# Optimization experiments

Measured on AMD Instinct MI355X. Metric: run time of the kernel, lower is better.

The kernel has to match this reference:

```python
import jax, jax.numpy as jnp
import numpy as np

B, C, H, W = 4, 256, 64, 64

def setup_inputs() -> dict:
    key = jax.random.key(0)
    k1, k2, k3, k4, k5, k6 = jax.random.split(key, 6)
    input_1 = jax.random.normal(k1, (B, C, H, W), dtype=jnp.float32)
    input_2 = jax.random.normal(k2, (B, C, H, W), dtype=jnp.float32)
    W_e = jax.random.normal(k3, (C, C), dtype=jnp.float32) * 0.02   # linear_e weight [out,in]
    gate_w = jax.random.normal(k4, (C,), dtype=jnp.float32) * 0.01  # Conv2d(c,1,1) weight squeezed
    W1 = jax.random.normal(k5, (C, 2 * C), dtype=jnp.float32) * 0.01  # final_conv_1 1x1 weight [out,in]
    W2 = jax.random.normal(k6, (C, 2 * C), dtype=jnp.float32) * 0.01  # final_conv_2
    return {"input_1": input_1, "input_2": input_2, "W_e": W_e,
            "gate_w": gate_w, "W1": W1, "W2": W2}

def reference(input_1, input_2, W_e, gate_w, W1, W2):
    b, c, h, w = input_1.shape
    hw = h * w
    ex = input_1.reshape(b, c, hw)   # exemplar_flat (b,c,n)
    q = input_2.reshape(b, c, hw)    # query_flat    (b,c,m)
    # linear_e on exemplar^T: (b,n,c) @ W_e^T -> (b,n,c)
    ec = jnp.einsum('bcn,dc->bnd', ex, W_e)
    # correlation A: (b,n,m)
    A = jnp.einsum('bnd,bdm->bnm', ec, q)
    A1 = jax.nn.softmax(A, axis=1)                       # softmax over exemplar pixels n
    Bmat = jax.nn.softmax(jnp.swapaxes(A, 1, 2), axis=1)  # (b,m,n), softmax over query pixels m
    query_att = jnp.einsum('bcn,bnm->bcm', ex, A1).reshape(b, c, h, w)
    exemplar_att = jnp.einsum('bcm,bmn->bcn', q, Bmat).reshape(b, c, h, w)
    # gate: 1x1 conv to 1 channel + sigmoid + elementwise mul
    m1 = jax.nn.sigmoid(jnp.einsum('bchw,c->bhw', exemplar_att, gate_w))[:, None]
    m2 = jax.nn.sigmoid(jnp.einsum('bchw,c->bhw', query_att, gate_w))[:, None]
    att1 = jnp.concatenate([exemplar_att * m1, input_1], axis=1)  # (b,2c,h,w)
    att2 = jnp.concatenate([query_att * m2, input_2], axis=1)
    out1 = jnp.einsum('bkhw,ok->bohw', att1, W1)
    out2 = jnp.einsum('bkhw,ok->bohw', att2, W2)
    return out1, out2
```

## Files before the change

kernel.cpp:

```cpp
#include <hip/hip_runtime.h>
#include <cstdint>
#include <cstddef>

#define BATCH 4
#define CCH   256
#define HW    4096
#define NM    4096

typedef __attribute__((ext_vector_type(8))) short s16x8;
typedef __attribute__((ext_vector_type(4))) float f32x4;

__device__ __forceinline__ short f2bf(float f) {
    unsigned u = __float_as_uint(f);
    u += 0x7FFFu + ((u >> 16) & 1u);
    return (short)(u >> 16);
}
__device__ __forceinline__ float bf2f(short s) {
    return __uint_as_float(((unsigned)(unsigned short)s) << 16);
}

__global__ __launch_bounds__(256) void k_cast(const float* __restrict__ s,
                                              short* __restrict__ d, int n) {
    int i = (blockIdx.x * 256 + threadIdx.x) * 4;
    if (i + 3 < n) {
        float4 v = *(const float4*)&s[i];
        *(short4*)&d[i] = make_short4(f2bf(v.x), f2bf(v.y), f2bf(v.z), f2bf(v.w));
    }
}

__global__ __launch_bounds__(256) void k_prep(const float* __restrict__ in1,
                                              const float* __restrict__ in2,
                                              short* __restrict__ X16,
                                              short* __restrict__ Q16,
                                              short* __restrict__ Xt16,
                                              short* __restrict__ Qt16) {
    __shared__ short S[64][72];
    int t = threadIdx.x;
    int p0 = blockIdx.x * 64, c0 = blockIdx.y * 64;
    int z = blockIdx.z;
    int b = z >> 1, which = z & 1;
    const float* src = (which ? in2 : in1) + (size_t)b * CCH * HW;
    short* direct = (which ? Q16 : X16) + (size_t)b * CCH * HW;
    short* trans  = (which ? Qt16 : Xt16) + (size_t)b * HW * CCH;
    int tx = t & 15, ty = t >> 4;
#pragma unroll
    for (int i = 0; i < 4; ++i) {
        int c = ty + i * 16;
        float4 v = *(const float4*)&src[(size_t)(c0 + c) * HW + p0 + tx * 4];
        short4 h = make_short4(f2bf(v.x), f2bf(v.y), f2bf(v.z), f2bf(v.w));
        *(short4*)&direct[(size_t)(c0 + c) * HW + p0 + tx * 4] = h;
        S[tx * 4 + 0][c] = h.x;
        S[tx * 4 + 1][c] = h.y;
        S[tx * 4 + 2][c] = h.z;
        S[tx * 4 + 3][c] = h.w;
    }
    __syncthreads();
#pragma unroll
    for (int i = 0; i < 4; ++i) {
        int p = ty + i * 16;
        short4 v = *(const short4*)&S[p][tx * 4];
        *(short4*)&trans[(size_t)(p0 + p) * CCH + c0 + tx * 4] = v;
    }
}

__global__ __launch_bounds__(256) void k_E_mfma(const short* __restrict__ Xt16,
                                                const short* __restrict__ We16,
                                                short* __restrict__ E16n) {
    __shared__ short As[128 * 72];
    __shared__ short Bs[128 * 72];
    int t = threadIdx.x;
    int d0 = blockIdx.x * 128, n0 = blockIdx.y * 128, b = blockIdx.z;
    const short* Xb = Xt16 + (size_t)b * HW * CCH;
    short* Eb = E16n + (size_t)b * HW * CCH;
    int lm = t & 15, q = (t >> 4) & 3, w = t >> 6;
    int wr = (w >> 1) * 64, wc = (w & 1) * 64;
    f32x4 acc[4][4];
#pragma unroll
    for (int i = 0; i < 4; ++i)
#pragma unroll
        for (int j = 0; j < 4; ++j) acc[i][j] = (f32x4){0.f, 0.f, 0.f, 0.f};

    for (int k0 = 0; k0 < CCH; k0 += 64) {
#pragma unroll
        for (int u = 0; u < 4; ++u) {
            int chunk = t + u * 256;
            int row = chunk >> 3, off = (chunk & 7) * 8;
            *(float4*)&As[row * 72 + off] =
                *(const float4*)&Xb[(size_t)(n0 + row) * CCH + k0 + off];
            *(float4*)&Bs[row * 72 + off] =
                *(const float4*)&We16[(size_t)(d0 + row) * CCH + k0 + off];
        }
        __syncthreads();
#pragma unroll
        for (int kk = 0; kk < 2; ++kk) {
            s16x8 af[4], bfr[4];
#pragma unroll
            for (int i = 0; i < 4; ++i)
                af[i] = *(const s16x8*)&As[(wr + i * 16 + lm) * 72 + kk * 32 + q * 8];
#pragma unroll
            for (int j = 0; j < 4; ++j)
                bfr[j] = *(const s16x8*)&Bs[(wc + j * 16 + lm) * 72 + kk * 32 + q * 8];
#pragma unroll
            for (int i = 0; i < 4; ++i)
#pragma unroll
                for (int j = 0; j < 4; ++j)
                    acc[i][j] = __builtin_amdgcn_mfma_f32_16x16x32_bf16(
                        af[i], bfr[j], acc[i][j], 0, 0, 0);
        }
        __syncthreads();
    }
#pragma unroll
    for (int i = 0; i < 4; ++i)
#pragma unroll
        for (int r = 0; r < 4; ++r) {
            size_t base = (size_t)(n0 + wr + i * 16 + q * 4 + r) * CCH;
#pragma unroll
            for (int j = 0; j < 4; ++j)
                Eb[base + d0 + wc + j * 16 + lm] = f2bf(acc[i][j][r]);
        }
}

__global__ __launch_bounds__(512, 2) void k_fused(const short* __restrict__ E16n,
                                                  const short* __restrict__ Qt16,
                                                  const short* __restrict__ Q16,
                                                  const short* __restrict__ X16,
                                                  const float* __restrict__ gw,
                                                  short* __restrict__ eattT,
                                                  short* __restrict__ qattT,
                                                  float* __restrict__ m1v,
                                                  float* __restrict__ m2v) {
    __shared__ short ArS[128 * 264];
    __shared__ short Ps[2][128 * 136];
    __shared__ float rs[8 * 128];
    __shared__ float grs[8 * 128];

    int t = threadIdx.x;
    int gid = blockIdx.x;
    int unit = gid & 7;
    int b = unit >> 1, which = unit & 1;
    int r0 = (gid >> 3) * 128;

    const short* Ar = (which ? Qt16 : E16n) + (size_t)b * HW * CCH;
    const short* Ac = (which ? E16n : Qt16) + (size_t)b * HW * CCH;
    const short* V  = (which ? X16  : Q16 ) + (size_t)b * CCH * HW;
    short* Out = (which ? qattT : eattT) + (size_t)b * HW * CCH;
    float* mdst = (which ? m2v : m1v) + (size_t)b * HW;

    int lm = t & 15, q = (t >> 4) & 3, w = t >> 6;
    int wqs = w * 16;
    int cq  = w * 32;

    float gwv[2];
#pragma unroll
    for (int j = 0; j < 2; ++j) gwv[j] = gw[cq + j * 16 + lm];

#pragma unroll
    for (int u = 0; u < 8; ++u) {
        int chunk = t + u * 512;
        int row = chunk >> 5, off = (chunk & 31) * 8;
        *(float4*)&ArS[row * 264 + off] =
            *(const float4*)&Ar[(size_t)(r0 + row) * CCH + off];
    }
    __syncthreads();

    f32x4 oacc[8][2];
    float rsum[8][4];
#pragma unroll
    for (int i = 0; i < 8; ++i) {
#pragma unroll
        for (int j = 0; j < 2; ++j) oacc[i][j] = (f32x4){0.f, 0.f, 0.f, 0.f};
#pragma unroll
        for (int r = 0; r < 4; ++r) rsum[i][r] = 0.f;
    }

    int buf = 0;
    for (int col0 = 0; col0 < NM; col0 += 128, buf ^= 1) {
        f32x4 sacc[8];
#pragma unroll
        for (int i = 0; i < 8; ++i) sacc[i] = (f32x4){0.f, 0.f, 0.f, 0.f};
#pragma unroll
        for (int kk = 0; kk < 8; ++kk) {
            s16x8 af[8], bf;
#pragma unroll
            for (int i = 0; i < 8; ++i)
                af[i] = *(const s16x8*)&ArS[(i * 16 + lm) * 264 + kk * 32 + q * 8];
            bf = *(const s16x8*)&Ac[(size_t)(col0 + wqs + lm) * CCH + kk * 32 + q * 8];
#pragma unroll
            for (int i = 0; i < 8; ++i)
                sacc[i] = __builtin_amdgcn_mfma_f32_16x16x32_bf16(
                    af[i], bf, sacc[i], 0, 0, 0);
        }
#pragma unroll
        for (int i = 0; i < 8; ++i)
#pragma unroll
            for (int r = 0; r < 4; ++r) {
                float v = bf2f(f2bf(__expf(sacc[i][r])));
                rsum[i][r] += v;
                sacc[i][r] = v;
            }
#pragma unroll
        for (int i = 0; i < 8; ++i)
#pragma unroll
            for (int r = 0; r < 4; ++r)
                Ps[buf][(i * 16 + q * 4 + r) * 136 + wqs + lm] =
                    (short)(__float_as_uint(sacc[i][r]) >> 16);
        __syncthreads();
#pragma unroll
        for (int km = 0; km < 4; ++km) {
            s16x8 pf[8], vf[2];
#pragma unroll
            for (int j = 0; j < 2; ++j)
                vf[j] = *(const s16x8*)&V[(size_t)(cq + j * 16 + lm) * HW +
                                          col0 + km * 32 + q * 8];
#pragma unroll
            for (int i = 0; i < 8; ++i)
                pf[i] = *(const s16x8*)&Ps[buf][(i * 16 + lm) * 136 + km * 32 + q * 8];
#pragma unroll
            for (int i = 0; i < 8; ++i)
#pragma unroll
                for (int j = 0; j < 2; ++j)
                    oacc[i][j] = __builtin_amdgcn_mfma_f32_16x16x32_bf16(
                        pf[i], vf[j], oacc[i][j], 0, 0, 0);
        }
    }

#pragma unroll
    for (int i = 0; i < 8; ++i)
#pragma unroll
        for (int r = 0; r < 4; ++r) {
            float s = rsum[i][r];
            s += __shfl_xor(s, 1, 64);
            s += __shfl_xor(s, 2, 64);
            s += __shfl_xor(s, 4, 64);
            s += __shfl_xor(s, 8, 64);
            if (lm == 0) rs[w * 128 + i * 16 + q * 4 + r] = s;
        }
    __syncthreads();

    float gacc[8][4];
#pragma unroll
    for (int i = 0; i < 8; ++i)
#pragma unroll
        for (int r = 0; r < 4; ++r) {
            int row = i * 16 + q * 4 + r;
            float tot = 0.f;
#pragma unroll
            for (int ww = 0; ww < 8; ++ww) tot += rs[ww * 128 + row];
            float inv = 1.f / tot;
            size_t base = (size_t)(r0 + row) * CCH;
            float ga = 0.f;
#pragma unroll
            for (int j = 0; j < 2; ++j) {
                short h = f2bf(oacc[i][j][r] * inv);
                Out[base + cq + j * 16 + lm] = h;
                ga = fmaf(bf2f(h), gwv[j], ga);
            }
            gacc[i][r] = ga;
        }
#pragma unroll
    for (int i = 0; i < 8; ++i)
#pragma unroll
        for (int r = 0; r < 4; ++r) {
            float s = gacc[i][r];
            s += __shfl_xor(s, 1, 64);
            s += __shfl_xor(s, 2, 64);
            s += __shfl_xor(s, 4, 64);
            s += __shfl_xor(s, 8, 64);
            if (lm == 0) grs[w * 128 + i * 16 + q * 4 + r] = s;
        }
    __syncthreads();
    if (t < 128) {
        float g = 0.f;
#pragma unroll
        for (int ww = 0; ww < 8; ++ww) g += grs[ww * 128 + t];
        mdst[r0 + t] = 1.f / (1.f + __expf(-g));
    }
}

__global__ __launch_bounds__(256) void k_final(const short* __restrict__ W16_1,
                                               const short* __restrict__ W16_2,
                                               const short* __restrict__ eattT,
                                               const short* __restrict__ qattT,
                                               const short* __restrict__ Xt16,
                                               const short* __restrict__ Qt16,
                                               const float* __restrict__ m1v,
                                               const float* __restrict__ m2v,
                                               float* __restrict__ outbase) {
    __shared__ short As[128 * 40];
    __shared__ short Bs[64 * 40];
    int t = threadIdx.x;
    int zz = blockIdx.z;
    int half = zz >> 2, b = zz & 3;
    const short* W16 = half ? W16_2 : W16_1;
    const short* attT = (half ? qattT : eattT);
    const short* inT  = (half ? Qt16 : Xt16);
    const float* gate = half ? m2v : m1v;
    float* outp = outbase + (size_t)half * BATCH * CCH * HW;
    int p0 = blockIdx.x * 64, o0 = blockIdx.y * 128;
    const short* Tb0 = attT + (size_t)b * HW * CCH;
    const short* Tb1 = inT + (size_t)b * HW * CCH;
    int lm = t & 15, q = (t >> 4) & 3, w = t >> 6;
    int wr = (w >> 1) * 64, wc = (w & 1) * 32;
    f32x4 acc[2][4][2];
#pragma unroll
    for (int ph = 0; ph < 2; ++ph)
#pragma unroll
        for (int i = 0; i < 4; ++i)
#pragma unroll
            for (int j = 0; j < 2; ++j) acc[ph][i][j] = (f32x4){0.f, 0.f, 0.f, 0.f};

    int brow = t >> 2, boff = (t & 3) * 8;
    for (int ph = 0; ph < 2; ++ph) {
        const short* Tb = ph ? Tb1 : Tb0;
        for (int k0 = 0; k0 < CCH; k0 += 32) {
#pragma unroll
            for (int u = 0; u < 2; ++u) {
                int chunk = t + u * 256;
                int row = chunk >> 2, off = (chunk & 3) * 8;
                *(float4*)&As[row * 40 + off] =
                    *(const float4*)&W16[(size_t)(o0 + row) * 512 + ph * 256 + k0 + off];
            }
            *(float4*)&Bs[brow * 40 + boff] =
                *(const float4*)&Tb[(size_t)(p0 + brow) * CCH + k0 + boff];
            __syncthreads();
            s16x8 af[4], bfr[2];
#pragma unroll
            for (int i = 0; i < 4; ++i)
                af[i] = *(const s16x8*)&As[(wr + i * 16 + lm) * 40 + q * 8];
#pragma unroll
            for (int j = 0; j < 2; ++j)
                bfr[j] = *(const s16x8*)&Bs[(wc + j * 16 + lm) * 40 + q * 8];
#pragma unroll
            for (int i = 0; i < 4; ++i)
#pragma unroll
                for (int j = 0; j < 2; ++j)
                    acc[ph][i][j] = __builtin_amdgcn_mfma_f32_16x16x32_bf16(
                        af[i], bfr[j], acc[ph][i][j], 0, 0, 0);
            __syncthreads();
        }
    }
#pragma unroll
    for (int j = 0; j < 2; ++j) {
        int p = p0 + wc + j * 16 + lm;
        float gv = gate[(size_t)b * HW + p];
#pragma unroll
        for (int i = 0; i < 4; ++i)
#pragma unroll
            for (int r = 0; r < 4; ++r) {
                int o = o0 + wr + i * 16 + q * 4 + r;
                outp[((size_t)b * CCH + o) * HW + p] =
                    acc[0][i][j][r] * gv + acc[1][i][j][r];
            }
    }
}

extern "C" void kernel_launch(void* const* d_in, const int* in_sizes, int n_in,
                              void* d_out, int out_size, void* d_ws, size_t ws_size,
                              hipStream_t stream) {
    (void)in_sizes; (void)n_in; (void)out_size; (void)ws_size;
    const float* in1 = (const float*)d_in[0];
    const float* in2 = (const float*)d_in[1];
    const float* We  = (const float*)d_in[2];
    const float* gw  = (const float*)d_in[3];
    const float* W1  = (const float*)d_in[4];
    const float* W2  = (const float*)d_in[5];
    float* out = (float*)d_out;
    char* ws = (char*)d_ws;

    const size_t SB = (size_t)BATCH * CCH * HW * 2;
    const size_t WB = (size_t)CCH * 2 * CCH * 2;
    const size_t EB = (size_t)CCH * CCH * 2;
    const size_t VB = (size_t)BATCH * NM * 4;

    size_t off = 0;
    auto alloc = [&](size_t bytes) {
        char* p = ws + off;
        off += (bytes + 255) & ~(size_t)255;
        return p;
    };
    short* W16_1 = (short*)alloc(WB);
    short* W16_2 = (short*)alloc(WB);
    short* We16  = (short*)alloc(EB);
    short* Xt16  = (short*)alloc(SB);
    short* Qt16  = (short*)alloc(SB);
    short* E16n  = (short*)alloc(SB);
    short* eattT = (short*)alloc(SB);
    short* qattT = (short*)alloc(SB);
    short* X16   = (short*)alloc(SB);
    short* Q16   = (short*)alloc(SB);
    float* m1v   = (float*)alloc(VB);
    float* m2v   = (float*)alloc(VB);

    const int nW = CCH * 2 * CCH;
    const int nWe = CCH * CCH;

    k_cast<<<dim3(nW / 1024), 256, 0, stream>>>(W1, W16_1, nW);
    k_cast<<<dim3(nW / 1024), 256, 0, stream>>>(W2, W16_2, nW);
    k_cast<<<dim3(nWe / 1024), 256, 0, stream>>>(We, We16, nWe);
    k_prep<<<dim3(HW / 64, CCH / 64, 8), 256, 0, stream>>>(in1, in2, X16, Q16,
                                                           Xt16, Qt16);

    k_E_mfma<<<dim3(2, 32, BATCH), 256, 0, stream>>>(Xt16, We16, E16n);

    k_fused<<<dim3((HW / 128) * 8), 512, 0, stream>>>(E16n, Qt16, Q16, X16, gw,
                                                      eattT, qattT, m1v, m2v);

    k_final<<<dim3(64, 2, 8), 256, 0, stream>>>(W16_1, W16_2, eattT, qattT,
                                                Xt16, Qt16, m1v, m2v, out);
}
```

Measured before the change: 303.9 us.

## Keep query rows in registers and async-prefetch swizzled key tiles into LDS

```diff
diff --git a/kernel.cpp b/kernel.cpp
--- a/kernel.cpp
+++ b/kernel.cpp
@@ -17,6 +17,12 @@
 }
 __device__ __forceinline__ float bf2f(short s) {
     return __uint_as_float(((unsigned)(unsigned short)s) << 16);
+}
+
+__device__ __forceinline__ void gload16(const void* g, void* l) {
+    __builtin_amdgcn_global_load_lds(
+        (const __attribute__((address_space(1))) unsigned int*)g,
+        (__attribute__((address_space(3))) unsigned int*)l, 16, 0, 0);
 }
 
 __global__ __launch_bounds__(256) void k_cast(const float* __restrict__ s,
@@ -129,9 +135,9 @@
                                                   short* __restrict__ qattT,
                                                   float* __restrict__ m1v,
                                                   float* __restrict__ m2v) {
-    __shared__ short ArS[128 * 264];
-    __shared__ short Ps[2][128 * 136];
-    __shared__ float rs[8 * 128];
+    __shared__ short AcS[128 * 256];
+    __shared__ short Ps[128 * 264];
+    __shared__ float rs[128];
     __shared__ float grs[8 * 128];
 
     int t = threadIdx.x;
@@ -147,94 +153,117 @@
     float* mdst = (which ? m2v : m1v) + (size_t)b * HW;
 
     int lm = t & 15, q = (t >> 4) & 3, w = t >> 6;
-    int wqs = w * 16;
-    int cq  = w * 32;
+    int lane = t & 63;
+    int cq = w * 32;
 
     float gwv[2];
 #pragma unroll
     for (int j = 0; j < 2; ++j) gwv[j] = gw[cq + j * 16 + lm];
 
-#pragma unroll
-    for (int u = 0; u < 8; ++u) {
-        int chunk = t + u * 512;
-        int row = chunk >> 5, off = (chunk & 31) * 8;
-        *(float4*)&ArS[row * 264 + off] =
-            *(const float4*)&Ar[(size_t)(r0 + row) * CCH + off];
+    s16x8 af[8];
+#pragma unroll
+    for (int kk = 0; kk < 8; ++kk)
+        af[kk] = *(const s16x8*)&Ar[(size_t)(r0 + w * 16 + lm) * CCH + kk * 32 + q * 8];
+
+    {
+        const char* AcB = (const char*)Ac;
+#pragma unroll
+        for (int c = 0; c < 8; ++c) {
+            int Lb = (w * 8 + c) << 10;
+            int L = Lb + lane * 16;
+            int col = L >> 9;
+            int soff = (col << 9) | ((L & 511) ^ ((col & 7) << 4));
+            gload16(AcB + soff, (char*)AcS + Lb);
+        }
     }
     __syncthreads();
 
     f32x4 oacc[8][2];
-    float rsum[8][4];
-#pragma unroll
-    for (int i = 0; i < 8; ++i) {
+    float rsum[4];
+#pragma unroll
+    for (int i = 0; i < 8; ++i)
 #pragma unroll
         for (int j = 0; j < 2; ++j) oacc[i][j] = (f32x4){0.f, 0.f, 0.f, 0.f};
 #pragma unroll
-        for (int r = 0; r < 4; ++r) rsum[i][r] = 0.f;
-    }
-
-    int buf = 0;
-    for (int col0 = 0; col0 < NM; col0 += 128, buf ^= 1) {
+    for (int r = 0; r < 4; ++r) rsum[r] = 0.f;
+
+    for (int col0 = 0; col0 < NM; col0 += 128) {
+        s16x8 vf[4][2];
+#pragma unroll
+        for (int km = 0; km < 4; ++km)
+#pragma unroll
+            for (int j = 0; j < 2; ++j)
+                vf[km][j] = *(const s16x8*)&V[(size_t)(cq + j * 16 + lm) * HW +
+                                              col0 + km * 32 + q * 8];
+
         f32x4 sacc[8];
 #pragma unroll
-        for (int i = 0; i < 8; ++i) sacc[i] = (f32x4){0.f, 0.f, 0.f, 0.f};
+        for (int j = 0; j < 8; ++j) sacc[j] = (f32x4){0.f, 0.f, 0.f, 0.f};
 #pragma unroll
         for (int kk = 0; kk < 8; ++kk) {
-            s16x8 af[8], bf;
+            int swk = ((kk * 64 + q * 16) ^ ((lm & 7) << 4)) >> 1;
+            s16x8 bf[8];
+#pragma unroll
+            for (int j = 0; j < 8; ++j)
+                bf[j] = *(const s16x8*)&AcS[(j * 16 + lm) * 256 + swk];
+#pragma unroll
+            for (int j = 0; j < 8; ++j)
+                sacc[j] = __builtin_amdgcn_mfma_f32_16x16x32_bf16(
+                    af[kk], bf[j], sacc[j], 0, 0, 0);
+        }
+#pragma unroll
+        for (int j = 0; j < 8; ++j)
+#pragma unroll
+            for (int r = 0; r < 4; ++r) {
+                float v = bf2f(f2bf(__expf(sacc[j][r])));
+                rsum[r] += v;
+                sacc[j][r] = v;
+            }
+#pragma unroll
+        for (int j = 0; j < 8; ++j)
+#pragma unroll
+            for (int r = 0; r < 4; ++r)
+                Ps[(w * 16 + q * 4 + r) * 264 + j * 16 + lm] =
+                    (short)(__float_as_uint(sacc[j][r]) >> 16);
+        __syncthreads();
+
+        if (col0 + 128 < NM) {
+            const char* AcB = (const char*)(Ac + (size_t)(col0 + 128) * CCH);
+#pragma unroll
+            for (int c = 0; c < 8; ++c) {
+                int Lb = (w * 8 + c) << 10;
+                int L = Lb + lane * 16;
+                int col = L >> 9;
+                int soff = (col << 9) | ((L & 511) ^ ((col & 7) << 4));
+                gload16(AcB + soff, (char*)AcS + Lb);
+            }
+        }
+
+#pragma unroll
+        for (int km = 0; km < 4; ++km) {
+            s16x8 pf[8];
 #pragma unroll
             for (int i = 0; i < 8; ++i)
-                af[i] = *(const s16x8*)&ArS[(i * 16 + lm) * 264 + kk * 32 + q * 8];
-            bf = *(const s16x8*)&Ac[(size_t)(col0 + wqs + lm) * CCH + kk * 32 + q * 8];
-#pragma unroll
-            for (int i = 0; i < 8; ++i)
-                sacc[i] = __builtin_amdgcn_mfma_f32_16x16x32_bf16(
-                    af[i], bf, sacc[i], 0, 0, 0);
-        }
-#pragma unroll
-        for (int i = 0; i < 8; ++i)
-#pragma unroll
-            for (int r = 0; r < 4; ++r) {
-                float v = bf2f(f2bf(__expf(sacc[i][r])));
-                rsum[i][r] += v;
-                sacc[i][r] = v;
-            }
-#pragma unroll
-        for (int i = 0; i < 8; ++i)
-#pragma unroll
-            for (int r = 0; r < 4; ++r)
-                Ps[buf][(i * 16 + q * 4 + r) * 136 + wqs + lm] =
-                    (short)(__float_as_uint(sacc[i][r]) >> 16);
-        __syncthreads();
-#pragma unroll
-        for (int km = 0; km < 4; ++km) {
-            s16x8 pf[8], vf[2];
-#pragma unroll
-            for (int j = 0; j < 2; ++j)
-                vf[j] = *(const s16x8*)&V[(size_t)(cq + j * 16 + lm) * HW +
-                                          col0 + km * 32 + q * 8];
-#pragma unroll
-            for (int i = 0; i < 8; ++i)
-                pf[i] = *(const s16x8*)&Ps[buf][(i * 16 + lm) * 136 + km * 32 + q * 8];
+                pf[i] = *(const s16x8*)&Ps[(i * 16 + lm) * 264 + km * 32 + q * 8];
 #pragma unroll
             for (int i = 0; i < 8; ++i)
 #pragma unroll
                 for (int j = 0; j < 2; ++j)
                     oacc[i][j] = __builtin_amdgcn_mfma_f32_16x16x32_bf16(
-                        pf[i], vf[j], oacc[i][j], 0, 0, 0);
-        }
-    }
-
-#pragma unroll
-    for (int i = 0; i < 8; ++i)
-#pragma unroll
-        for (int r = 0; r < 4; ++r) {
-            float s = rsum[i][r];
-            s += __shfl_xor(s, 1, 64);
-            s += __shfl_xor(s, 2, 64);
-            s += __shfl_xor(s, 4, 64);
-            s += __shfl_xor(s, 8, 64);
-            if (lm == 0) rs[w * 128 + i * 16 + q * 4 + r] = s;
-        }
+                        pf[i], vf[km][j], oacc[i][j], 0, 0, 0);
+        }
+        __syncthreads();
+    }
+
+#pragma unroll
+    for (int r = 0; r < 4; ++r) {
+        float s = rsum[r];
+        s += __shfl_xor(s, 1, 64);
+        s += __shfl_xor(s, 2, 64);
+        s += __shfl_xor(s, 4, 64);
+        s += __shfl_xor(s, 8, 64);
+        if (lm == 0) rs[w * 16 + q * 4 + r] = s;
+    }
     __syncthreads();
 
     float gacc[8][4];
@@ -243,10 +272,7 @@
 #pragma unroll
         for (int r = 0; r < 4; ++r) {
             int row = i * 16 + q * 4 + r;
-            float tot = 0.f;
-#pragma unroll
-            for (int ww = 0; ww < 8; ++ww) tot += rs[ww * 128 + row];
-            float inv = 1.f / tot;
+            float inv = 1.f / rs[row];
             size_t base = (size_t)(r0 + row) * CCH;
             float ga = 0.f;
 #pragma unroll
```

Result: faster. 295.7 us (-2.7%).
